# Optimization experiments

Measured on AMD Instinct MI355X. Metric: run time of the kernel, lower is better.

Reference implementation:

```python
import jax, jax.numpy as jnp
import numpy as np

MICRO_BATCHES = 2
TOP_K = 2
D = 512
E = 8  # num_experts (world_size=1 -> all local)
B, S = 8, 8192


def setup_inputs() -> dict:
    key = jax.random.key(0)
    ks = jax.random.split(key, 12)
    s = 0.02
    return {
        "x": jax.random.normal(ks[0], (B, S, D), dtype=jnp.float32),
        "ln_g": jnp.ones((D,), jnp.float32),
        "ln_b": jnp.zeros((D,), jnp.float32),
        "attn_w": jax.random.normal(ks[1], (D, D), jnp.float32) * s,
        "attn_b": jnp.zeros((D,), jnp.float32),
        "gate_w": jax.random.normal(ks[2], (E, D), jnp.float32) * s,
        "fc1_w": jax.random.normal(ks[3], (E, 4 * D, D), jnp.float32) * s,
        "fc1_b": jnp.zeros((E, 4 * D), jnp.float32),
        "fc2_w": jax.random.normal(ks[4], (E, D, 4 * D), jnp.float32) * s,
        "fc2_b": jnp.zeros((E, D), jnp.float32),
        "next_w": jax.random.normal(ks[5], (D, D), jnp.float32) * s,
        "next_b": jnp.zeros((D,), jnp.float32),
    }


def reference(x, ln_g, ln_b, attn_w, attn_b, gate_w, fc1_w, fc1_b, fc2_w, fc2_b, next_w, next_b):
    b, s, d = x.shape
    xf = x.reshape(b * s, d)
    # attn_norm -> attn linear + residual
    mu = jnp.mean(xf, axis=-1, keepdims=True)
    var = jnp.var(xf, axis=-1, keepdims=True)
    normed = (xf - mu) / jnp.sqrt(var + 1e-5) * ln_g + ln_b
    x_attn = normed @ attn_w.T + attn_b + xf
    # gating: logits + top-k (computed in the original but unused for the output path)
    logits = x_attn @ gate_w.T
    _scores, _indices = jax.lax.top_k(logits, TOP_K)
    # dispatch (identity all_to_all at world_size=1): tokens split positionally
    # into MICRO_BATCHES micro-batches, each chunked into E equal expert slices
    e = fc1_w.shape[0]
    t = (b * s) // (MICRO_BATCHES * e)  # tokens per expert per micro-batch
    tok = x_attn.reshape(MICRO_BATCHES, e, t, d)  # [m,e,t,d]
    h = jnp.einsum("meti,ehi->meth", tok, fc1_w) + fc1_b[None, :, None, :]
    h = jax.nn.gelu(h, approximate=False)  # torch nn.GELU default = erf
    y = jnp.einsum("meth,edh->metd", h, fc2_w) + fc2_b[None, :, None, :]
    # combine (identity) + next_layer_ops (Linear -> GELU), order preserved by cat
    yf = y.reshape(b * s, d)
    out = jax.nn.gelu(yf @ next_w.T + next_b, approximate=False)
    return out.reshape(b, s, d)
```

## Files before the change

kernel.cpp:

```cpp
#include <hip/hip_runtime.h>
#include <math.h>

typedef __bf16 bf16x8 __attribute__((ext_vector_type(8)));
typedef float f32x4 __attribute__((ext_vector_type(4)));
typedef unsigned short us4v __attribute__((ext_vector_type(4)));
typedef unsigned short us8v __attribute__((ext_vector_type(8)));

#define NTOK 65536
#define DMODEL 512

__device__ __forceinline__ unsigned short f2bf(float f) {
  unsigned int u = __float_as_uint(f);
  u += 0x7fffu + ((u >> 16) & 1u);
  return (unsigned short)(u >> 16);
}

__device__ __forceinline__ float gelu_fast(float x) {
  float x3 = x * x * x;
  float u = __expf(1.5957691216057308f * (x + 0.044715f * x3));
  return x * __fdividef(u, u + 1.0f);
}

__device__ __forceinline__ void async16(const void* g, void* l) {
  __builtin_amdgcn_global_load_lds((const __attribute__((address_space(1))) void*)g,
                                   (__attribute__((address_space(3))) void*)l,
                                   16, 0, 0);
}

__global__ __launch_bounds__(256) void cvt_bf16_kernel(const float4* __restrict__ in,
                                                       us4v* __restrict__ out, int n4) {
  int i = blockIdx.x * 256 + threadIdx.x;
  if (i < n4) {
    float4 v = in[i];
    us4v o;
    o.x = f2bf(v.x); o.y = f2bf(v.y); o.z = f2bf(v.z); o.w = f2bf(v.w);
    out[i] = o;
  }
}

__global__ __launch_bounds__(256) void ln_kernel(const float* __restrict__ x,
                                                 const float* __restrict__ g,
                                                 const float* __restrict__ b,
                                                 unsigned short* __restrict__ out) {
  const int w = threadIdx.x >> 6;
  const int lane = threadIdx.x & 63;
  const size_t row = (size_t)blockIdx.x * 4 + w;
  const float4* xv = (const float4*)(x + row * DMODEL);
  float4 v0 = xv[lane * 2];
  float4 v1 = xv[lane * 2 + 1];
  float s  = v0.x + v0.y + v0.z + v0.w + v1.x + v1.y + v1.z + v1.w;
  float ss = v0.x*v0.x + v0.y*v0.y + v0.z*v0.z + v0.w*v0.w
           + v1.x*v1.x + v1.y*v1.y + v1.z*v1.z + v1.w*v1.w;
#pragma unroll
  for (int m = 1; m < 64; m <<= 1) {
    s  += __shfl_xor(s, m, 64);
    ss += __shfl_xor(ss, m, 64);
  }
  const float mean = s * (1.0f / DMODEL);
  const float var  = ss * (1.0f / DMODEL) - mean * mean;
  const float rstd = rsqrtf(var + 1e-5f);
  const int c = lane * 8;
  const float4* gv = (const float4*)(g + c);
  const float4* bv = (const float4*)(b + c);
  float4 g0 = gv[0], g1 = gv[1], bb0 = bv[0], bb1 = bv[1];
  us8v o;
  o[0] = f2bf((v0.x - mean) * rstd * g0.x + bb0.x);
  o[1] = f2bf((v0.y - mean) * rstd * g0.y + bb0.y);
  o[2] = f2bf((v0.z - mean) * rstd * g0.z + bb0.z);
  o[3] = f2bf((v0.w - mean) * rstd * g0.w + bb0.w);
  o[4] = f2bf((v1.x - mean) * rstd * g1.x + bb1.x);
  o[5] = f2bf((v1.y - mean) * rstd * g1.y + bb1.y);
  o[6] = f2bf((v1.z - mean) * rstd * g1.z + bb1.z);
  o[7] = f2bf((v1.w - mean) * rstd * g1.w + bb1.w);
  *(us8v*)(out + row * DMODEL + c) = o;
}

template <int EPI, bool EXPERT, typename OutT, int K>
__global__ __launch_bounds__(256, 2) void gemm_bt2(
    const unsigned short* __restrict__ A, const unsigned short* __restrict__ B,
    const float* __restrict__ bias, const float* __restrict__ resid,
    OutT* __restrict__ C, int N) {
  __shared__ alignas(16) unsigned short tA[128 * 64];
  __shared__ alignas(16) unsigned short tB[128 * 64];
  const int tid = threadIdx.x;
  const int w = tid >> 6;
  const int lane = tid & 63;
  const int wm = w & 1, wn = w >> 1;
  const int quad = lane >> 4, lm = lane & 15;

  const int ncol = N >> 7;
  const int perx = gridDim.x >> 3;
  const int xcd = blockIdx.x & 7;
  const int wk = xcd * perx + (blockIdx.x >> 3);
  const int band_rows = (ncol == 16) ? 8 : 16;
  const int bb = band_rows * ncol;
  const int band = wk / bb;
  const int rem = wk - band * bb;
  const int ct = rem / band_rows;
  const int rib = rem - ct * band_rows;
  const size_t row0 = (size_t)(band * band_rows + rib) * 128;
  const int col0 = ct * 128;

  const unsigned short* Bp = B;
  const float* biasp = bias;
  if (EXPERT) {
    const int e = (int)((row0 >> 12) & 7);
    Bp += (size_t)e * (size_t)N * (size_t)K;
    biasp += (size_t)e * (size_t)N;
  }

  const unsigned short* gA[4];
  const unsigned short* gB[4];
  unsigned short* lA[4];
  unsigned short* lB[4];
#pragma unroll
  for (int j = 0; j < 4; ++j) {
    const int c = w * 4 + j;
    const int f = c * 64 + lane;
    const int r = f >> 3;
    const int u = f & 7;
    const int kg = u ^ (r & 7);
    gA[j] = A + (row0 + (size_t)r) * (size_t)K + kg * 8;
    gB[j] = Bp + ((size_t)col0 + (size_t)r) * (size_t)K + kg * 8;
    lA[j] = tA + c * 512;
    lB[j] = tB + c * 512;
  }

  f32x4 acc[4][4] = {};

  for (int k0 = 0; k0 < K; k0 += 64) {
#pragma unroll
    for (int j = 0; j < 4; ++j) {
      async16(gA[j], lA[j]);
      async16(gB[j], lB[j]);
      gA[j] += 64;
      gB[j] += 64;
    }
    __syncthreads();
    bf16x8 af[2][4], bfr[2][4];
#pragma unroll
    for (int s = 0; s < 2; ++s) {
#pragma unroll
      for (int mi = 0; mi < 4; ++mi) {
        const int r = wm * 64 + mi * 16 + lm;
        af[s][mi] = *(const bf16x8*)&tA[(r * 8 + ((s * 4 + quad) ^ (r & 7))) * 8];
      }
#pragma unroll
      for (int ni = 0; ni < 4; ++ni) {
        const int cc = wn * 64 + ni * 16 + lm;
        bfr[s][ni] = *(const bf16x8*)&tB[(cc * 8 + ((s * 4 + quad) ^ (cc & 7))) * 8];
      }
    }
#pragma unroll
    for (int s = 0; s < 2; ++s)
#pragma unroll
      for (int mi = 0; mi < 4; ++mi)
#pragma unroll
        for (int ni = 0; ni < 4; ++ni)
          acc[mi][ni] =
              __builtin_amdgcn_mfma_f32_16x16x32_bf16(af[s][mi], bfr[s][ni], acc[mi][ni], 0, 0, 0);
    __syncthreads();
  }

#pragma unroll
  for (int mi = 0; mi < 4; ++mi) {
#pragma unroll
    for (int ni = 0; ni < 4; ++ni) {
      const int col = col0 + wn * 64 + ni * 16 + lm;
      const float bv = biasp[col];
#pragma unroll
      for (int r = 0; r < 4; ++r) {
        const size_t grow = row0 + (size_t)(wm * 64 + mi * 16 + quad * 4 + r);
        float v = acc[mi][ni][r] + bv;
        if constexpr (EPI == 0) v += resid[grow * (size_t)N + col];
        if constexpr (EPI == 1) v = gelu_fast(v);
        if constexpr (sizeof(OutT) == 4) {
          C[grow * (size_t)N + col] = v;
        } else {
          C[grow * (size_t)N + col] = (OutT)f2bf(v);
        }
      }
    }
  }
}

extern "C" void kernel_launch(void* const* d_in, const int* in_sizes, int n_in,
                              void* d_out, int out_size, void* d_ws, size_t ws_size,
                              hipStream_t stream) {
  const float* x      = (const float*)d_in[0];
  const float* ln_g   = (const float*)d_in[1];
  const float* ln_b   = (const float*)d_in[2];
  const float* attn_w = (const float*)d_in[3];
  const float* attn_b = (const float*)d_in[4];
  const float* fc1_w  = (const float*)d_in[6];
  const float* fc1_b  = (const float*)d_in[7];
  const float* fc2_w  = (const float*)d_in[8];
  const float* fc2_b  = (const float*)d_in[9];
  const float* next_w = (const float*)d_in[10];
  const float* next_b = (const float*)d_in[11];

  char* ws = (char*)d_ws;
  const size_t MB = 1024ull * 1024ull;
  unsigned short* wN    = (unsigned short*)(ws);
  unsigned short* wXat  = (unsigned short*)(ws + 64 * MB);
  unsigned short* wH    = (unsigned short*)(ws + 128 * MB);
  unsigned short* attnbf = (unsigned short*)(ws + 384 * MB);
  unsigned short* fc1bf  = (unsigned short*)(ws + 385 * MB);
  unsigned short* fc2bf  = (unsigned short*)(ws + 401 * MB);
  unsigned short* nextbf = (unsigned short*)(ws + 417 * MB);

  {
    int n4;
    n4 = (512 * 512) / 4;
    cvt_bf16_kernel<<<dim3((n4 + 255) / 256), dim3(256), 0, stream>>>((const float4*)attn_w, (us4v*)attnbf, n4);
    n4 = (8 * 2048 * 512) / 4;
    cvt_bf16_kernel<<<dim3((n4 + 255) / 256), dim3(256), 0, stream>>>((const float4*)fc1_w, (us4v*)fc1bf, n4);
    n4 = (8 * 512 * 2048) / 4;
    cvt_bf16_kernel<<<dim3((n4 + 255) / 256), dim3(256), 0, stream>>>((const float4*)fc2_w, (us4v*)fc2bf, n4);
    n4 = (512 * 512) / 4;
    cvt_bf16_kernel<<<dim3((n4 + 255) / 256), dim3(256), 0, stream>>>((const float4*)next_w, (us4v*)nextbf, n4);
  }

  ln_kernel<<<dim3(NTOK / 4), dim3(256), 0, stream>>>(x, ln_g, ln_b, wN);

  gemm_bt2<0, false, unsigned short, 512><<<dim3((NTOK / 128) * 4), dim3(256), 0, stream>>>(
      wN, attnbf, attn_b, x, wXat, 512);

  gemm_bt2<1, true, unsigned short, 512><<<dim3((NTOK / 128) * 16), dim3(256), 0, stream>>>(
      wXat, fc1bf, fc1_b, nullptr, wH, 2048);

  gemm_bt2<2, true, unsigned short, 2048><<<dim3((NTOK / 128) * 4), dim3(256), 0, stream>>>(
      wH, fc2bf, fc2_b, nullptr, wN, 512);

  gemm_bt2<1, false, float, 512><<<dim3((NTOK / 128) * 4), dim3(256), 0, stream>>>(
      wN, nextbf, next_b, nullptr, (float*)d_out, 512);
}
```

Baseline: 802.8 us.

## Replace GEMM with 256x256-tile, 8-wave, double-buffered ping-pong pipelined kernel

Replaces the 128x128, 4-wave GEMM with a 256x256 tile computed by 512 threads (8 waves). The K loop is double-buffered in LDS, with async global-to-LDS loads for tile t+2 issued while MFMAs run on tile t. The MFMA work is split into four quadrants separated by barriers, with s_setprio raised around each MFMA block and explicit vmcnt/lgkmcnt waits. The goal is to hide load latency and raise arithmetic intensity per tile, at the cost of 128KB of LDS per block, a larger accumulator register set, and fewer blocks in the grid.

New measurement: 803.3 us. No clear change (+0.1%).

```diff
diff --git a/kernel.cpp b/kernel.cpp
--- a/kernel.cpp
+++ b/kernel.cpp
@@ -75,31 +75,42 @@
   *(us8v*)(out + row * DMODEL + c) = o;
 }
 
+#define MFMA_Q(mh, nh)                                                           \
+  {                                                                              \
+    _Pragma("unroll") for (int s = 0; s < 2; ++s)                                \
+        _Pragma("unroll") for (int mi = 0; mi < 4; ++mi)                         \
+            _Pragma("unroll") for (int ni = 0; ni < 2; ++ni)                     \
+                acc[(mh) * 4 + mi][(nh) * 2 + ni] =                              \
+        __builtin_amdgcn_mfma_f32_16x16x32_bf16(af[s][(mh) * 4 + mi],            \
+                                                bfr[s][(nh) * 2 + ni],           \
+                                                acc[(mh) * 4 + mi][(nh) * 2 + ni],\
+                                                0, 0, 0);                        \
+  }
+
 template <int EPI, bool EXPERT, typename OutT, int K>
-__global__ __launch_bounds__(256, 2) void gemm_bt2(
+__global__ __launch_bounds__(512, 2) void gemm8p(
     const unsigned short* __restrict__ A, const unsigned short* __restrict__ B,
     const float* __restrict__ bias, const float* __restrict__ resid,
     OutT* __restrict__ C, int N) {
-  __shared__ alignas(16) unsigned short tA[128 * 64];
-  __shared__ alignas(16) unsigned short tB[128 * 64];
+  __shared__ alignas(16) unsigned short lds[2][2][16384];
   const int tid = threadIdx.x;
   const int w = tid >> 6;
   const int lane = tid & 63;
-  const int wm = w & 1, wn = w >> 1;
+  const int wm = w >> 2, wn = w & 3;
   const int quad = lane >> 4, lm = lane & 15;
 
-  const int ncol = N >> 7;
+  const int ncol = N >> 8;
   const int perx = gridDim.x >> 3;
   const int xcd = blockIdx.x & 7;
   const int wk = xcd * perx + (blockIdx.x >> 3);
-  const int band_rows = (ncol == 16) ? 8 : 16;
+  const int band_rows = (K == 2048) ? 2 : (ncol >= 8 ? 4 : 8);
   const int bb = band_rows * ncol;
   const int band = wk / bb;
   const int rem = wk - band * bb;
   const int ct = rem / band_rows;
   const int rib = rem - ct * band_rows;
-  const size_t row0 = (size_t)(band * band_rows + rib) * 128;
-  const int col0 = ct * 128;
+  const size_t row0 = (size_t)(band * band_rows + rib) * 256;
+  const int col0 = ct * 256;
 
   const unsigned short* Bp = B;
   const float* biasp = bias;
@@ -109,68 +120,119 @@
     biasp += (size_t)e * (size_t)N;
   }
 
-  const unsigned short* gA[4];
-  const unsigned short* gB[4];
-  unsigned short* lA[4];
-  unsigned short* lB[4];
-#pragma unroll
-  for (int j = 0; j < 4; ++j) {
-    const int c = w * 4 + j;
-    const int f = c * 64 + lane;
-    const int r = f >> 3;
-    const int u = f & 7;
-    const int kg = u ^ (r & 7);
-    gA[j] = A + (row0 + (size_t)r) * (size_t)K + kg * 8;
-    gB[j] = Bp + ((size_t)col0 + (size_t)r) * (size_t)K + kg * 8;
-    lA[j] = tA + c * 512;
-    lB[j] = tB + c * 512;
-  }
-
-  f32x4 acc[4][4] = {};
-
-  for (int k0 = 0; k0 < K; k0 += 64) {
-#pragma unroll
-    for (int j = 0; j < 4; ++j) {
-      async16(gA[j], lA[j]);
-      async16(gB[j], lB[j]);
-      gA[j] += 64;
-      gB[j] += 64;
-    }
-    __syncthreads();
-    bf16x8 af[2][4], bfr[2][4];
+  const int r0 = w * 32 + (lane >> 3);
+  const int kg0 = (lane & 7) ^ (lane >> 3);
+  const unsigned short* gA = A + (row0 + (size_t)r0) * (size_t)K + kg0 * 8;
+  const unsigned short* gB = Bp + ((size_t)col0 + (size_t)r0) * (size_t)K + kg0 * 8;
+
+  auto stageA = [&](int buf, const unsigned short* p) {
+    unsigned short* l = &lds[buf][0][(w * 4) * 512];
+    async16(p, l);
+    async16(p + 8 * K, l + 512);
+    async16(p + 16 * K, l + 1024);
+    async16(p + 24 * K, l + 1536);
+  };
+  auto stageB = [&](int buf, const unsigned short* p) {
+    unsigned short* l = &lds[buf][1][(w * 4) * 512];
+    async16(p, l);
+    async16(p + 8 * K, l + 512);
+    async16(p + 16 * K, l + 1024);
+    async16(p + 24 * K, l + 1536);
+  };
+
+  f32x4 acc[8][4] = {};
+  const int NT = K / 64;
+
+  stageA(0, gA);
+  stageB(0, gB);
+  stageA(1, gA + 64);
+  stageB(1, gB + 64);
+  gA += 128;
+  gB += 128;
+  asm volatile("s_waitcnt vmcnt(8)" ::: "memory");
+  __builtin_amdgcn_s_barrier();
+
+  for (int t = 0; t < NT; ++t) {
+    const unsigned short* tA = &lds[t & 1][0][0];
+    const unsigned short* tB = &lds[t & 1][1][0];
+    const bool st = (t + 2 < NT);
+    bf16x8 af[2][8], bfr[2][4];
+
 #pragma unroll
     for (int s = 0; s < 2; ++s) {
 #pragma unroll
       for (int mi = 0; mi < 4; ++mi) {
-        const int r = wm * 64 + mi * 16 + lm;
+        const int r = wm * 128 + mi * 16 + lm;
         af[s][mi] = *(const bf16x8*)&tA[(r * 8 + ((s * 4 + quad) ^ (r & 7))) * 8];
       }
 #pragma unroll
-      for (int ni = 0; ni < 4; ++ni) {
-        const int cc = wn * 64 + ni * 16 + lm;
-        bfr[s][ni] = *(const bf16x8*)&tB[(cc * 8 + ((s * 4 + quad) ^ (cc & 7))) * 8];
-      }
-    }
-#pragma unroll
-    for (int s = 0; s < 2; ++s)
-#pragma unroll
-      for (int mi = 0; mi < 4; ++mi)
-#pragma unroll
-        for (int ni = 0; ni < 4; ++ni)
-          acc[mi][ni] =
-              __builtin_amdgcn_mfma_f32_16x16x32_bf16(af[s][mi], bfr[s][ni], acc[mi][ni], 0, 0, 0);
-    __syncthreads();
-  }
-
-#pragma unroll
-  for (int mi = 0; mi < 4; ++mi) {
+      for (int ni = 0; ni < 2; ++ni) {
+        const int c = wn * 64 + ni * 16 + lm;
+        bfr[s][ni] = *(const bf16x8*)&tB[(c * 8 + ((s * 4 + quad) ^ (c & 7))) * 8];
+      }
+    }
+    __builtin_amdgcn_s_barrier();
+    asm volatile("s_waitcnt lgkmcnt(0)" ::: "memory");
+    __builtin_amdgcn_s_setprio(1);
+    MFMA_Q(0, 0);
+    __builtin_amdgcn_s_setprio(0);
+    __builtin_amdgcn_s_barrier();
+
+#pragma unroll
+    for (int s = 0; s < 2; ++s) {
+#pragma unroll
+      for (int mi = 0; mi < 4; ++mi) {
+        const int r = wm * 128 + (mi + 4) * 16 + lm;
+        af[s][mi + 4] = *(const bf16x8*)&tA[(r * 8 + ((s * 4 + quad) ^ (r & 7))) * 8];
+      }
+#pragma unroll
+      for (int ni = 0; ni < 2; ++ni) {
+        const int c = wn * 64 + (ni + 2) * 16 + lm;
+        bfr[s][ni + 2] = *(const bf16x8*)&tB[(c * 8 + ((s * 4 + quad) ^ (c & 7))) * 8];
+      }
+    }
+    __builtin_amdgcn_s_barrier();
+    asm volatile("s_waitcnt lgkmcnt(0)" ::: "memory");
+    __builtin_amdgcn_s_setprio(1);
+    MFMA_Q(0, 1);
+    __builtin_amdgcn_s_setprio(0);
+    __builtin_amdgcn_s_barrier();
+
+    if (st) stageA(t & 1, gA);
+    __builtin_amdgcn_s_barrier();
+    __builtin_amdgcn_s_setprio(1);
+    MFMA_Q(1, 0);
+    __builtin_amdgcn_s_setprio(0);
+    __builtin_amdgcn_s_barrier();
+
+    if (st) {
+      stageB(t & 1, gB);
+      gA += 64;
+      gB += 64;
+    }
+    __builtin_amdgcn_s_barrier();
+    __builtin_amdgcn_s_setprio(1);
+    MFMA_Q(1, 1);
+    __builtin_amdgcn_s_setprio(0);
+
+    if (t < NT - 2) {
+      asm volatile("s_waitcnt vmcnt(8)" ::: "memory");
+      __builtin_amdgcn_s_barrier();
+    } else if (t == NT - 2) {
+      asm volatile("s_waitcnt vmcnt(0)" ::: "memory");
+      __builtin_amdgcn_s_barrier();
+    }
+  }
+
+#pragma unroll
+  for (int mi = 0; mi < 8; ++mi) {
 #pragma unroll
     for (int ni = 0; ni < 4; ++ni) {
       const int col = col0 + wn * 64 + ni * 16 + lm;
       const float bv = biasp[col];
 #pragma unroll
       for (int r = 0; r < 4; ++r) {
-        const size_t grow = row0 + (size_t)(wm * 64 + mi * 16 + quad * 4 + r);
+        const size_t grow = row0 + (size_t)(wm * 128 + mi * 16 + quad * 4 + r);
         float v = acc[mi][ni][r] + bv;
         if constexpr (EPI == 0) v += resid[grow * (size_t)N + col];
         if constexpr (EPI == 1) v = gelu_fast(v);
@@ -223,15 +285,15 @@
 
   ln_kernel<<<dim3(NTOK / 4), dim3(256), 0, stream>>>(x, ln_g, ln_b, wN);
 
-  gemm_bt2<0, false, unsigned short, 512><<<dim3((NTOK / 128) * 4), dim3(256), 0, stream>>>(
+  gemm8p<0, false, unsigned short, 512><<<dim3((NTOK / 256) * 2), dim3(512), 0, stream>>>(
       wN, attnbf, attn_b, x, wXat, 512);
 
-  gemm_bt2<1, true, unsigned short, 512><<<dim3((NTOK / 128) * 16), dim3(256), 0, stream>>>(
+  gemm8p<1, true, unsigned short, 512><<<dim3((NTOK / 256) * 8), dim3(512), 0, stream>>>(
       wXat, fc1bf, fc1_b, nullptr, wH, 2048);
 
-  gemm_bt2<2, true, unsigned short, 2048><<<dim3((NTOK / 128) * 4), dim3(256), 0, stream>>>(
+  gemm8p<2, true, unsigned short, 2048><<<dim3((NTOK / 256) * 2), dim3(512), 0, stream>>>(
       wH, fc2bf, fc2_b, nullptr, wN, 512);
 
-  gemm_bt2<1, false, float, 512><<<dim3((NTOK / 128) * 4), dim3(256), 0, stream>>>(
+  gemm8p<1, false, float, 512><<<dim3((NTOK / 256) * 2), dim3(512), 0, stream>>>(
       wN, nextbf, next_b, nullptr, (float*)d_out, 512);
 }
```

## Double-buffer LDS tiles in GEMM to overlap global loads with MFMA

Applied to the files above, without the earlier changes.

Turns the single-buffered GEMM main loop into a two-stage ping-pong: the next K-tile is loaded asynchronously into the alternate LDS buffer while MFMAs run on the current one. One barrier per iteration replaces the previous pair of __syncthreads. Wave priority is raised around the MFMA block. LDS use doubles to 64 KB per block, which may limit the two-blocks-per-CU occupancy target.

Result: slower. 864.7 us (+7.7%).

```diff
diff --git a/kernel.cpp b/kernel.cpp
--- a/kernel.cpp
+++ b/kernel.cpp
@@ -76,12 +76,12 @@
 }
 
 template <int EPI, bool EXPERT, typename OutT, int K>
-__global__ __launch_bounds__(256, 2) void gemm_bt2(
+__global__ __launch_bounds__(256, 2) void gemm_bt3(
     const unsigned short* __restrict__ A, const unsigned short* __restrict__ B,
     const float* __restrict__ bias, const float* __restrict__ resid,
     OutT* __restrict__ C, int N) {
-  __shared__ alignas(16) unsigned short tA[128 * 64];
-  __shared__ alignas(16) unsigned short tB[128 * 64];
+  __shared__ alignas(16) unsigned short tA[2][128 * 64];
+  __shared__ alignas(16) unsigned short tB[2][128 * 64];
   const int tid = threadIdx.x;
   const int w = tid >> 6;
   const int lane = tid & 63;
@@ -111,8 +111,7 @@
 
   const unsigned short* gA[4];
   const unsigned short* gB[4];
-  unsigned short* lA[4];
-  unsigned short* lB[4];
+  int lo[4];
 #pragma unroll
   for (int j = 0; j < 4; ++j) {
     const int c = w * 4 + j;
@@ -122,35 +121,48 @@
     const int kg = u ^ (r & 7);
     gA[j] = A + (row0 + (size_t)r) * (size_t)K + kg * 8;
     gB[j] = Bp + ((size_t)col0 + (size_t)r) * (size_t)K + kg * 8;
-    lA[j] = tA + c * 512;
-    lB[j] = tB + c * 512;
+    lo[j] = c * 512;
   }
 
   f32x4 acc[4][4] = {};
-
-  for (int k0 = 0; k0 < K; k0 += 64) {
-#pragma unroll
-    for (int j = 0; j < 4; ++j) {
-      async16(gA[j], lA[j]);
-      async16(gB[j], lB[j]);
-      gA[j] += 64;
-      gB[j] += 64;
+  const int NT = K / 64;
+
+#pragma unroll
+  for (int j = 0; j < 4; ++j) {
+    async16(gA[j], &tA[0][lo[j]]);
+    async16(gB[j], &tB[0][lo[j]]);
+    gA[j] += 64;
+    gB[j] += 64;
+  }
+  asm volatile("s_waitcnt vmcnt(0)" ::: "memory");
+  __builtin_amdgcn_s_barrier();
+
+  for (int t = 0; t < NT; ++t) {
+    const int cur = t & 1;
+    if (t + 1 < NT) {
+#pragma unroll
+      for (int j = 0; j < 4; ++j) {
+        async16(gA[j], &tA[cur ^ 1][lo[j]]);
+        async16(gB[j], &tB[cur ^ 1][lo[j]]);
+        gA[j] += 64;
+        gB[j] += 64;
+      }
     }
-    __syncthreads();
     bf16x8 af[2][4], bfr[2][4];
 #pragma unroll
     for (int s = 0; s < 2; ++s) {
 #pragma unroll
       for (int mi = 0; mi < 4; ++mi) {
         const int r = wm * 64 + mi * 16 + lm;
-        af[s][mi] = *(const bf16x8*)&tA[(r * 8 + ((s * 4 + quad) ^ (r & 7))) * 8];
+        af[s][mi] = *(const bf16x8*)&tA[cur][(r * 8 + ((s * 4 + quad) ^ (r & 7))) * 8];
       }
 #pragma unroll
       for (int ni = 0; ni < 4; ++ni) {
         const int cc = wn * 64 + ni * 16 + lm;
-        bfr[s][ni] = *(const bf16x8*)&tB[(cc * 8 + ((s * 4 + quad) ^ (cc & 7))) * 8];
+        bfr[s][ni] = *(const bf16x8*)&tB[cur][(cc * 8 + ((s * 4 + quad) ^ (cc & 7))) * 8];
       }
     }
+    __builtin_amdgcn_s_setprio(1);
 #pragma unroll
     for (int s = 0; s < 2; ++s)
 #pragma unroll
@@ -159,7 +171,9 @@
         for (int ni = 0; ni < 4; ++ni)
           acc[mi][ni] =
               __builtin_amdgcn_mfma_f32_16x16x32_bf16(af[s][mi], bfr[s][ni], acc[mi][ni], 0, 0, 0);
-    __syncthreads();
+    __builtin_amdgcn_s_setprio(0);
+    asm volatile("s_waitcnt vmcnt(0)" ::: "memory");
+    __builtin_amdgcn_s_barrier();
   }
 
 #pragma unroll
@@ -223,15 +237,15 @@
 
   ln_kernel<<<dim3(NTOK / 4), dim3(256), 0, stream>>>(x, ln_g, ln_b, wN);
 
-  gemm_bt2<0, false, unsigned short, 512><<<dim3((NTOK / 128) * 4), dim3(256), 0, stream>>>(
+  gemm_bt3<0, false, unsigned short, 512><<<dim3((NTOK / 128) * 4), dim3(256), 0, stream>>>(
       wN, attnbf, attn_b, x, wXat, 512);
 
-  gemm_bt2<1, true, unsigned short, 512><<<dim3((NTOK / 128) * 16), dim3(256), 0, stream>>>(
+  gemm_bt3<1, true, unsigned short, 512><<<dim3((NTOK / 128) * 16), dim3(256), 0, stream>>>(
       wXat, fc1bf, fc1_b, nullptr, wH, 2048);
 
-  gemm_bt2<2, true, unsigned short, 2048><<<dim3((NTOK / 128) * 4), dim3(256), 0, stream>>>(
+  gemm_bt3<2, true, unsigned short, 2048><<<dim3((NTOK / 128) * 4), dim3(256), 0, stream>>>(
       wH, fc2bf, fc2_b, nullptr, wN, 512);
 
-  gemm_bt2<1, false, float, 512><<<dim3((NTOK / 128) * 4), dim3(256), 0, stream>>>(
+  gemm_bt3<1, false, float, 512><<<dim3((NTOK / 128) * 4), dim3(256), 0, stream>>>(
       wN, nextbf, next_b, nullptr, (float*)d_out, 512);
 }
```

## Halve GEMM K-tile to 32 and raise occupancy to four blocks per CU

Applied to the files above, without the earlier changes.

The bf16 MFMA GEMM now stages a 128x32 K-slice per iteration instead of 128x64. This halves LDS use per block and lets launch bounds request four resident blocks per CU. The swizzle and load mapping are reworked for 4 chunks per row, and s_setprio is raised around the MFMA burst so math waves get priority. The trade-off is twice as many loop iterations and barriers per output tile, with less work between syncs and a tighter register budget at the higher occupancy.

New measurement: 854.3 us. +6.4%, slower.

```diff
diff --git a/kernel.cpp b/kernel.cpp
--- a/kernel.cpp
+++ b/kernel.cpp
@@ -76,12 +76,12 @@
 }
 
 template <int EPI, bool EXPERT, typename OutT, int K>
-__global__ __launch_bounds__(256, 2) void gemm_bt2(
+__global__ __launch_bounds__(256, 4) void gemm_bt4(
     const unsigned short* __restrict__ A, const unsigned short* __restrict__ B,
     const float* __restrict__ bias, const float* __restrict__ resid,
     OutT* __restrict__ C, int N) {
-  __shared__ alignas(16) unsigned short tA[128 * 64];
-  __shared__ alignas(16) unsigned short tB[128 * 64];
+  __shared__ alignas(16) unsigned short tA[128 * 32];
+  __shared__ alignas(16) unsigned short tB[128 * 32];
   const int tid = threadIdx.x;
   const int w = tid >> 6;
   const int lane = tid & 63;
@@ -109,56 +109,49 @@
     biasp += (size_t)e * (size_t)N;
   }
 
-  const unsigned short* gA[4];
-  const unsigned short* gB[4];
-  unsigned short* lA[4];
-  unsigned short* lB[4];
-#pragma unroll
-  for (int j = 0; j < 4; ++j) {
-    const int c = w * 4 + j;
-    const int f = c * 64 + lane;
-    const int r = f >> 3;
-    const int u = f & 7;
-    const int kg = u ^ (r & 7);
-    gA[j] = A + (row0 + (size_t)r) * (size_t)K + kg * 8;
-    gB[j] = Bp + ((size_t)col0 + (size_t)r) * (size_t)K + kg * 8;
-    lA[j] = tA + c * 512;
-    lB[j] = tB + c * 512;
+  const unsigned short* gA[2];
+  const unsigned short* gB[2];
+  int lo[2];
+  const int kg0 = (lane & 3) ^ ((lane >> 3) & 3);
+#pragma unroll
+  for (int j = 0; j < 2; ++j) {
+    const int c = w * 2 + j;
+    const int r = c * 16 + (lane >> 2);
+    gA[j] = A + (row0 + (size_t)r) * (size_t)K + kg0 * 8;
+    gB[j] = Bp + ((size_t)col0 + (size_t)r) * (size_t)K + kg0 * 8;
+    lo[j] = c * 512;
   }
 
   f32x4 acc[4][4] = {};
 
-  for (int k0 = 0; k0 < K; k0 += 64) {
-#pragma unroll
-    for (int j = 0; j < 4; ++j) {
-      async16(gA[j], lA[j]);
-      async16(gB[j], lB[j]);
-      gA[j] += 64;
-      gB[j] += 64;
+  for (int k0 = 0; k0 < K; k0 += 32) {
+#pragma unroll
+    for (int j = 0; j < 2; ++j) {
+      async16(gA[j], &tA[lo[j]]);
+      async16(gB[j], &tB[lo[j]]);
+      gA[j] += 32;
+      gB[j] += 32;
     }
     __syncthreads();
-    bf16x8 af[2][4], bfr[2][4];
-#pragma unroll
-    for (int s = 0; s < 2; ++s) {
-#pragma unroll
-      for (int mi = 0; mi < 4; ++mi) {
-        const int r = wm * 64 + mi * 16 + lm;
-        af[s][mi] = *(const bf16x8*)&tA[(r * 8 + ((s * 4 + quad) ^ (r & 7))) * 8];
-      }
-#pragma unroll
-      for (int ni = 0; ni < 4; ++ni) {
-        const int cc = wn * 64 + ni * 16 + lm;
-        bfr[s][ni] = *(const bf16x8*)&tB[(cc * 8 + ((s * 4 + quad) ^ (cc & 7))) * 8];
-      }
-    }
-#pragma unroll
-    for (int s = 0; s < 2; ++s)
-#pragma unroll
-      for (int mi = 0; mi < 4; ++mi)
-#pragma unroll
-        for (int ni = 0; ni < 4; ++ni)
-          acc[mi][ni] =
-              __builtin_amdgcn_mfma_f32_16x16x32_bf16(af[s][mi], bfr[s][ni], acc[mi][ni], 0, 0, 0);
+    bf16x8 af[4], bfr[4];
+#pragma unroll
+    for (int mi = 0; mi < 4; ++mi) {
+      const int r = wm * 64 + mi * 16 + lm;
+      af[mi] = *(const bf16x8*)&tA[(r * 4 + (quad ^ ((r >> 1) & 3))) * 8];
+    }
+#pragma unroll
+    for (int ni = 0; ni < 4; ++ni) {
+      const int cc = wn * 64 + ni * 16 + lm;
+      bfr[ni] = *(const bf16x8*)&tB[(cc * 4 + (quad ^ ((cc >> 1) & 3))) * 8];
+    }
+    __builtin_amdgcn_s_setprio(1);
+#pragma unroll
+    for (int mi = 0; mi < 4; ++mi)
+#pragma unroll
+      for (int ni = 0; ni < 4; ++ni)
+        acc[mi][ni] =
+            __builtin_amdgcn_mfma_f32_16x16x32_bf16(af[mi], bfr[ni], acc[mi][ni], 0, 0, 0);
+    __builtin_amdgcn_s_setprio(0);
     __syncthreads();
   }
 
@@ -223,15 +216,15 @@
 
   ln_kernel<<<dim3(NTOK / 4), dim3(256), 0, stream>>>(x, ln_g, ln_b, wN);
 
-  gemm_bt2<0, false, unsigned short, 512><<<dim3((NTOK / 128) * 4), dim3(256), 0, stream>>>(
+  gemm_bt4<0, false, unsigned short, 512><<<dim3((NTOK / 128) * 4), dim3(256), 0, stream>>>(
       wN, attnbf, attn_b, x, wXat, 512);
 
-  gemm_bt2<1, true, unsigned short, 512><<<dim3((NTOK / 128) * 16), dim3(256), 0, stream>>>(
+  gemm_bt4<1, true, unsigned short, 512><<<dim3((NTOK / 128) * 16), dim3(256), 0, stream>>>(
       wXat, fc1bf, fc1_b, nullptr, wH, 2048);
 
-  gemm_bt2<2, true, unsigned short, 2048><<<dim3((NTOK / 128) * 4), dim3(256), 0, stream>>>(
+  gemm_bt4<2, true, unsigned short, 2048><<<dim3((NTOK / 128) * 4), dim3(256), 0, stream>>>(
       wH, fc2bf, fc2_b, nullptr, wN, 512);
 
-  gemm_bt2<1, false, float, 512><<<dim3((NTOK / 128) * 4), dim3(256), 0, stream>>>(
+  gemm_bt4<1, false, float, 512><<<dim3((NTOK / 128) * 4), dim3(256), 0, stream>>>(
       wN, nextbf, next_b, nullptr, (float*)d_out, 512);
 }
```
